# Kernel optimization log

Hardware: AMD Instinct MI355X
Metric: run time of the kernel (lower is better)

Reference implementation:

```python
import jax, jax.numpy as jnp
import numpy as np


def setup_inputs() -> dict:
    key = jax.random.key(0)
    k1, k2, k3 = jax.random.split(key, 3)
    N, DIN, DOUT = 8192, 256, 256
    adjacency = jax.random.uniform(k1, (N, N), dtype=jnp.float32)
    input_feature = jax.random.normal(k2, (N, DIN), dtype=jnp.float32)
    weight = jax.random.normal(k3, (DIN, DOUT), dtype=jnp.float32) * (1.0 / np.sqrt(DIN))
    bias = jnp.zeros((DOUT,), dtype=jnp.float32)
    return {"adjacency": adjacency, "input_feature": input_feature,
            "weight": weight, "bias": bias, "l": 1}


def reference(adjacency, input_feature, weight, bias, l):
    # support = X @ W
    support = input_feature @ weight  # [N, DOUT]
    # A = adjacency + l*I ; degrees = rowsum(A) = rowsum(adjacency) + l
    deg = jnp.sum(adjacency, axis=1) + jnp.asarray(l, adjacency.dtype)  # [N]
    # D^{-1/2} with inf (from zero degree) replaced by 0
    d = jnp.where(deg > 0, deg ** -0.5, jnp.zeros_like(deg))  # [N]
    # D @ adjacency @ D  (row scale then col scale of the ORIGINAL adjacency,
    # self-loops only affect the degree, matching the torch code)
    norm_adj = adjacency * d[:, None] * d[None, :]  # [N, N]
    out = norm_adj @ support + bias  # [N, DOUT]
    return out
```

## Files before the change

kernel.cpp:

```cpp
#include <hip/hip_runtime.h>
#include <hip/hip_bf16.h>


typedef __attribute__((ext_vector_type(8))) short short8;
typedef __attribute__((ext_vector_type(4))) float f32x4;

#define NN 8192
#define DD 256

__device__ inline unsigned short f2bfu(float x) {
    unsigned int u = __builtin_bit_cast(unsigned int, x);
    u += 0x7fffu + ((u >> 16) & 1u);
    return (unsigned short)(u >> 16);
}
__device__ inline unsigned int f2bf2u(float x, float y) {
    return (unsigned int)f2bfu(x) | ((unsigned int)f2bfu(y) << 16);
}
__device__ inline short8 cvt8(float4 a, float4 b) {
    union { unsigned int i[4]; short8 s; } u;
    u.i[0] = f2bf2u(a.x, a.y);
    u.i[1] = f2bf2u(a.z, a.w);
    u.i[2] = f2bf2u(b.x, b.y);
    u.i[3] = f2bf2u(b.z, b.w);
    return u.s;
}

__global__ __launch_bounds__(256) void rowsum_kernel(const float* __restrict__ A,
                                                     const int* __restrict__ lp,
                                                     float* __restrict__ d) {
    const int row = blockIdx.x;
    const int t = threadIdx.x;
    const float4* Arow = (const float4*)(A + (size_t)row * NN);
    float s = 0.f;
#pragma unroll
    for (int it = 0; it < NN / 4 / 256; ++it) {
        float4 v = Arow[it * 256 + t];
        s += (v.x + v.y) + (v.z + v.w);
    }
#pragma unroll
    for (int off = 32; off > 0; off >>= 1) s += __shfl_down(s, off, 64);
    __shared__ float wsum[4];
    if ((t & 63) == 0) wsum[t >> 6] = s;
    __syncthreads();
    if (t == 0) {
        float deg = ((wsum[0] + wsum[1]) + (wsum[2] + wsum[3])) + (float)(*lp);
        d[row] = deg > 0.f ? rsqrtf(deg) : 0.f;
    }
}

__global__ __launch_bounds__(256) void wtrans_kernel(const float* __restrict__ W,
                                                     unsigned short* __restrict__ WT) {
    __shared__ unsigned short tile[64][65];
    const int tx = threadIdx.x & 63, ty = threadIdx.x >> 6;
    const int i0 = (blockIdx.x & 3) * 64;
    const int n0 = (blockIdx.x >> 2) * 64;
#pragma unroll
    for (int r = ty; r < 64; r += 4)
        tile[r][tx] = f2bfu(W[(size_t)(i0 + r) * DD + n0 + tx]);
    __syncthreads();
#pragma unroll
    for (int r = ty; r < 64; r += 4)
        WT[(size_t)(n0 + r) * DD + i0 + tx] = tile[tx][r];
}

__global__ __launch_bounds__(256) void support_kernel(const float* __restrict__ X,
                                                      const unsigned short* __restrict__ WT,
                                                      const float* __restrict__ d,
                                                      unsigned short* __restrict__ ST) {
    const int j0 = blockIdx.x * 16;
    const int lane = threadIdx.x & 63;
    const int w = threadIdx.x >> 6;
    const int q = lane >> 4;
    const int l15 = lane & 15;
    const int nb = w * 64;

    f32x4 acc[4];
#pragma unroll
    for (int b = 0; b < 4; ++b) acc[b] = (f32x4)(0.f);

    const float* Xbase = X + (size_t)(j0 + l15) * DD + q * 8;
    const unsigned short* Wbase = WT + (size_t)(nb + l15) * DD + q * 8;

#pragma unroll
    for (int k0 = 0; k0 < DD; k0 += 32) {
        const float4* p = (const float4*)(Xbase + k0);
        short8 afr = cvt8(p[0], p[1]);
        short8 bfr[4];
#pragma unroll
        for (int ni = 0; ni < 4; ++ni)
            bfr[ni] = *(const short8*)(Wbase + ni * 16 * DD + k0);
#pragma unroll
        for (int ni = 0; ni < 4; ++ni)
            acc[ni] = __builtin_amdgcn_mfma_f32_16x16x32_bf16(afr, bfr[ni], acc[ni], 0, 0, 0);
    }

    const int j0r = j0 + q * 4;
    float dj[4];
#pragma unroll
    for (int r = 0; r < 4; ++r) dj[r] = d[j0r + r];
#pragma unroll
    for (int ni = 0; ni < 4; ++ni) {
        const int n = nb + ni * 16 + l15;
        unsigned int lo = f2bf2u(acc[ni][0] * dj[0], acc[ni][1] * dj[1]);
        unsigned int hi = f2bf2u(acc[ni][2] * dj[2], acc[ni][3] * dj[3]);
        *(uint2*)(ST + (size_t)n * NN + j0r) = make_uint2(lo, hi);
    }
}

#define KCHUNK 1024
#define BK 64
#define NITER (KCHUNK / BK)
__global__ __launch_bounds__(256) void main_gemm(const float* __restrict__ A,
                                                 const unsigned short* __restrict__ ST,
                                                 const float* __restrict__ d,
                                                 const float* __restrict__ bias,
                                                 float* __restrict__ out) {
    __shared__ __align__(16) unsigned short Abuf[2][64][72];

    const int mt = blockIdx.x & 127;
    const int kc = blockIdx.x >> 7;
    const int m0 = mt * 64;
    const int kbeg = kc * KCHUNK;
    const int tid = threadIdx.x;
    const int lane = tid & 63;
    const int w = tid >> 6;
    const int q = lane >> 4;
    const int l15 = lane & 15;
    const int nb = w * 64;
    const int srow = tid >> 4;
    const int scol = (tid & 15) * 4;

    const float* Ast = A + (size_t)(m0 + srow) * NN + kbeg + scol;
    const unsigned short* Bbase = ST + (size_t)(nb + l15) * NN + kbeg + q * 8;

    f32x4 acc[4][4];
#pragma unroll
    for (int a = 0; a < 4; ++a)
#pragma unroll
        for (int b = 0; b < 4; ++b) acc[a][b] = (f32x4)(0.f);

    float4 nx[4];
#pragma unroll
    for (int p = 0; p < 4; ++p)
        nx[p] = *(const float4*)(Ast + (size_t)(p * 16) * NN);
#pragma unroll
    for (int p = 0; p < 4; ++p)
        *(uint2*)&Abuf[0][srow + p * 16][scol] =
            make_uint2(f2bf2u(nx[p].x, nx[p].y), f2bf2u(nx[p].z, nx[p].w));
    __syncthreads();

    for (int it = 0; it < NITER; ++it) {
        const int buf = it & 1;
        if (it + 1 < NITER) {
#pragma unroll
            for (int p = 0; p < 4; ++p)
                nx[p] = *(const float4*)(Ast + (size_t)(p * 16) * NN + (it + 1) * BK);
        }
#pragma unroll
        for (int kk = 0; kk < BK; kk += 32) {
            short8 afr[4], bfr[4];
#pragma unroll
            for (int mi = 0; mi < 4; ++mi)
                afr[mi] = *(const short8*)&Abuf[buf][mi * 16 + l15][kk + q * 8];
#pragma unroll
            for (int ni = 0; ni < 4; ++ni)
                bfr[ni] = *(const short8*)(Bbase + (size_t)(ni * 16) * NN + it * BK + kk);
#pragma unroll
            for (int mi = 0; mi < 4; ++mi)
#pragma unroll
                for (int ni = 0; ni < 4; ++ni)
                    acc[mi][ni] = __builtin_amdgcn_mfma_f32_16x16x32_bf16(afr[mi], bfr[ni], acc[mi][ni], 0, 0, 0);
        }
        if (it + 1 < NITER) {
            __syncthreads();
#pragma unroll
            for (int p = 0; p < 4; ++p)
                *(uint2*)&Abuf[buf ^ 1][srow + p * 16][scol] =
                    make_uint2(f2bf2u(nx[p].x, nx[p].y), f2bf2u(nx[p].z, nx[p].w));
            __syncthreads();
        }
    }

#pragma unroll
    for (int mi = 0; mi < 4; ++mi) {
        const int r0 = m0 + mi * 16 + q * 4;
        float dm[4];
#pragma unroll
        for (int r = 0; r < 4; ++r) dm[r] = d[r0 + r];
#pragma unroll
        for (int ni = 0; ni < 4; ++ni) {
            const int n = nb + ni * 16 + l15;
            const float bv = (kc == 0) ? bias[n] : 0.f;
#pragma unroll
            for (int r = 0; r < 4; ++r) {
                float val = acc[mi][ni][r] * dm[r] + bv;
                unsafeAtomicAdd(out + (size_t)(r0 + r) * DD + n, val);
            }
        }
    }
}

extern "C" void kernel_launch(void* const* d_in, const int* in_sizes, int n_in,
                              void* d_out, int out_size, void* d_ws, size_t ws_size,
                              hipStream_t stream) {
    const float* A = (const float*)d_in[0];
    const float* X = (const float*)d_in[1];
    const float* W = (const float*)d_in[2];
    const float* bias = (const float*)d_in[3];
    const int* lp = (const int*)d_in[4];
    float* out = (float*)d_out;

    float* d = (float*)d_ws;
    unsigned short* WT = (unsigned short*)((char*)d_ws + 32768);
    unsigned short* ST = (unsigned short*)((char*)d_ws + 32768 + 131072);

    (void)hipMemsetAsync(d_out, 0, (size_t)NN * DD * sizeof(float), stream);
    rowsum_kernel<<<NN, 256, 0, stream>>>(A, lp, d);
    wtrans_kernel<<<16, 256, 0, stream>>>(W, WT);
    support_kernel<<<NN / 16, 256, 0, stream>>>(X, WT, d, ST);
    main_gemm<<<128 * (NN / KCHUNK), 256, 0, stream>>>(A, ST, d, bias, out);
}
```

Measured before the change: 511.6 us.

## Deepen main GEMM prefetch pipeline with single barrier and larger K chunk

Restructures the main GEMM loop so the fp32 adjacency tiles are prefetched two iterations ahead in registers and the ST operand one iteration ahead. The two barriers per iteration become one raw s_barrier. Adjacency loads become nontemporal, and the K chunk per block doubles, halving block count and atomic output traffic. The aim is to hide global load latency in this bandwidth-bound streaming GEMM. The cost is more register pressure and fewer blocks for the GPU to spread across its compute units.

```diff
diff --git a/kernel.cpp b/kernel.cpp
--- a/kernel.cpp
+++ b/kernel.cpp
@@ -107,7 +107,7 @@
     }
 }
 
-#define KCHUNK 1024
+#define KCHUNK 2048
 #define BK 64
 #define NITER (KCHUNK / BK)
 __global__ __launch_bounds__(256) void main_gemm(const float* __restrict__ A,
@@ -131,7 +131,7 @@
     const int scol = (tid & 15) * 4;
 
     const float* Ast = A + (size_t)(m0 + srow) * NN + kbeg + scol;
-    const unsigned short* Bbase = ST + (size_t)(nb + l15) * NN + kbeg + q * 8;
+    const unsigned short* Bptr = ST + (size_t)(nb + l15) * NN + kbeg + q * 8;
 
     f32x4 acc[4][4];
 #pragma unroll
@@ -139,45 +139,66 @@
 #pragma unroll
         for (int b = 0; b < 4; ++b) acc[a][b] = (f32x4)(0.f);
 
-    float4 nx[4];
+    f32x4 r[2][4];
+    short8 bfr[2][2][4];
+
 #pragma unroll
     for (int p = 0; p < 4; ++p)
-        nx[p] = *(const float4*)(Ast + (size_t)(p * 16) * NN);
+        r[0][p] = __builtin_nontemporal_load((const f32x4*)(Ast + (size_t)(p * 16) * NN));
 #pragma unroll
     for (int p = 0; p < 4; ++p)
+        r[1][p] = __builtin_nontemporal_load((const f32x4*)(Ast + (size_t)(p * 16) * NN + BK));
+#pragma unroll
+    for (int kk2 = 0; kk2 < 2; ++kk2)
+#pragma unroll
+        for (int ni = 0; ni < 4; ++ni)
+            bfr[0][kk2][ni] = *(const short8*)(Bptr + (size_t)(ni * 16) * NN + kk2 * 32);
+#pragma unroll
+    for (int p = 0; p < 4; ++p) {
+        f32x4 v = r[0][p];
         *(uint2*)&Abuf[0][srow + p * 16][scol] =
-            make_uint2(f2bf2u(nx[p].x, nx[p].y), f2bf2u(nx[p].z, nx[p].w));
-    __syncthreads();
-
+            make_uint2(f2bf2u(v[0], v[1]), f2bf2u(v[2], v[3]));
+    }
+
+#pragma unroll 2
     for (int it = 0; it < NITER; ++it) {
         const int buf = it & 1;
+        __asm__ __volatile__("s_waitcnt lgkmcnt(0)\n\ts_barrier" ::: "memory");
+
         if (it + 1 < NITER) {
 #pragma unroll
+            for (int kk2 = 0; kk2 < 2; ++kk2)
+#pragma unroll
+                for (int ni = 0; ni < 4; ++ni)
+                    bfr[buf ^ 1][kk2][ni] =
+                        *(const short8*)(Bptr + (size_t)(ni * 16) * NN + (it + 1) * BK + kk2 * 32);
+        }
+        if (it + 2 < NITER) {
+#pragma unroll
             for (int p = 0; p < 4; ++p)
-                nx[p] = *(const float4*)(Ast + (size_t)(p * 16) * NN + (it + 1) * BK);
-        }
-#pragma unroll
-        for (int kk = 0; kk < BK; kk += 32) {
-            short8 afr[4], bfr[4];
+                r[buf][p] = __builtin_nontemporal_load(
+                    (const f32x4*)(Ast + (size_t)(p * 16) * NN + (it + 2) * BK));
+        }
+        if (it + 1 < NITER) {
+#pragma unroll
+            for (int p = 0; p < 4; ++p) {
+                f32x4 v = r[buf ^ 1][p];
+                *(uint2*)&Abuf[buf ^ 1][srow + p * 16][scol] =
+                    make_uint2(f2bf2u(v[0], v[1]), f2bf2u(v[2], v[3]));
+            }
+        }
+#pragma unroll
+        for (int kk2 = 0; kk2 < 2; ++kk2) {
+            short8 afr[4];
 #pragma unroll
             for (int mi = 0; mi < 4; ++mi)
-                afr[mi] = *(const short8*)&Abuf[buf][mi * 16 + l15][kk + q * 8];
-#pragma unroll
-            for (int ni = 0; ni < 4; ++ni)
-                bfr[ni] = *(const short8*)(Bbase + (size_t)(ni * 16) * NN + it * BK + kk);
+                afr[mi] = *(const short8*)&Abuf[buf][mi * 16 + l15][kk2 * 32 + q * 8];
 #pragma unroll
             for (int mi = 0; mi < 4; ++mi)
 #pragma unroll
                 for (int ni = 0; ni < 4; ++ni)
-                    acc[mi][ni] = __builtin_amdgcn_mfma_f32_16x16x32_bf16(afr[mi], bfr[ni], acc[mi][ni], 0, 0, 0);
-        }
-        if (it + 1 < NITER) {
-            __syncthreads();
-#pragma unroll
-            for (int p = 0; p < 4; ++p)
-                *(uint2*)&Abuf[buf ^ 1][srow + p * 16][scol] =
-                    make_uint2(f2bf2u(nx[p].x, nx[p].y), f2bf2u(nx[p].z, nx[p].w));
-            __syncthreads();
+                    acc[mi][ni] = __builtin_amdgcn_mfma_f32_16x16x32_bf16(
+                        afr[mi], bfr[buf][kk2][ni], acc[mi][ni], 0, 0, 0);
         }
     }
 
@@ -186,15 +207,15 @@
         const int r0 = m0 + mi * 16 + q * 4;
         float dm[4];
 #pragma unroll
-        for (int r = 0; r < 4; ++r) dm[r] = d[r0 + r];
+        for (int rr = 0; rr < 4; ++rr) dm[rr] = d[r0 + rr];
 #pragma unroll
         for (int ni = 0; ni < 4; ++ni) {
             const int n = nb + ni * 16 + l15;
             const float bv = (kc == 0) ? bias[n] : 0.f;
 #pragma unroll
-            for (int r = 0; r < 4; ++r) {
-                float val = acc[mi][ni][r] * dm[r] + bv;
-                unsafeAtomicAdd(out + (size_t)(r0 + r) * DD + n, val);
+            for (int rr = 0; rr < 4; ++rr) {
+                float val = acc[mi][ni][rr] * dm[rr] + bv;
+                unsafeAtomicAdd(out + (size_t)(r0 + rr) * DD + n, val);
             }
         }
     }
```

Result: faster. 482.4 us (-5.7%).
